# Kernel tuning notes

Hardware: AMD Instinct MI355X
Metric: run time of the kernel (lower is better)

## Reference

```python
import jax, jax.numpy as jnp
import numpy as np

N = 50000      # nodes
E = 800000     # edges (before self loops)
H = 4          # heads
C_IN = 128     # input feature dim
C_HID = 64     # per-head out channels (hidden_dim == output_dim)
SLOPE = 0.2    # GATConv leaky_relu negative slope


def setup_inputs() -> dict:
    key = jax.random.key(0)
    ks = jax.random.split(key, 16)
    x = jax.random.normal(ks[0], (N, C_IN), jnp.float32)
    edge_index = jax.random.randint(ks[1], (2, E), 0, N, jnp.int32)

    def p(k, shape):
        return jax.random.normal(k, shape, jnp.float32) * 0.05

    inp = {"x": x, "edge_index": edge_index}
    in_dims = [C_IN, C_HID, C_HID]
    for i in range(3):
        inp[f"W{i+1}"] = p(ks[2 + 4 * i], (in_dims[i], H * C_HID))
        inp[f"asrc{i+1}"] = p(ks[3 + 4 * i], (H, C_HID))
        inp[f"adst{i+1}"] = p(ks[4 + 4 * i], (H, C_HID))
        inp[f"b{i+1}"] = jnp.zeros((C_HID,), jnp.float32)
    return inp


def _gat_layer(x, src, dst, W, a_s, a_d, b):
    # x: [N, F_in]; src/dst: [E'] (self loops included)
    n = x.shape[0]
    h = (x @ W).reshape(n, H, -1)                      # [N, H, C]
    alpha_src = jnp.einsum('nhc,hc->nh', h, a_s)       # att_src . h  (source side)
    alpha_dst = jnp.einsum('nhc,hc->nh', h, a_d)       # att_dst . h  (target side)
    e = jax.nn.leaky_relu(alpha_src[src] + alpha_dst[dst], SLOPE)  # [E', H]
    # scatter-softmax over incoming edges of each dst node
    m = jax.ops.segment_max(e, dst, num_segments=n)    # [N, H]
    ex = jnp.exp(e - m[dst])
    denom = jax.ops.segment_sum(ex, dst, num_segments=n)
    alpha = ex / (denom[dst] + 1e-16)                  # [E', H]
    # scatter-add aggregation of weighted source features
    out = jax.ops.segment_sum(alpha[:, :, None] * h[src], dst, num_segments=n)  # [N, H, C]
    return out.mean(axis=1) + b                        # concat=False -> head mean, + bias


def reference(x, edge_index, W1, asrc1, adst1, b1, W2, asrc2, adst2, b2,
              W3, asrc3, adst3, b3):
    n = x.shape[0]
    loops = jnp.arange(n, dtype=edge_index.dtype)      # GATConv add_self_loops=True
    src = jnp.concatenate([edge_index[0], loops])
    dst = jnp.concatenate([edge_index[1], loops])
    for W, a_s, a_d, b in ((W1, asrc1, adst1, b1),
                           (W2, asrc2, adst2, b2),
                           (W3, asrc3, adst3, b3)):
        x = jax.nn.relu(_gat_layer(x, src, dst, W, a_s, a_d, b))
    return x
```

## Files before the change

kernel.cpp:

```cpp
#include <hip/hip_runtime.h>
#include <hip/hip_bf16.h>
#include <cstddef>

#define NH 4
#define CHID 64
#define HC 256

typedef __attribute__((ext_vector_type(8))) short bf16x8;
typedef __attribute__((ext_vector_type(4))) float f32x4;


__global__ void hist_kernel(const int* __restrict__ ei, int E, int N,
                            int* __restrict__ deg) {
  int i = blockIdx.x * blockDim.x + threadIdx.x;
  int EP = E + N;
  if (i >= EP) return;
  int d = (i < E) ? ei[E + i] : (i - E);
  atomicAdd(&deg[d], 1);
}

__global__ __launch_bounds__(256) void partial_sum_kernel(const int* __restrict__ deg,
                                                          int* __restrict__ part, int n) {
  __shared__ int red[4];
  int t = threadIdx.x;
  int i = blockIdx.x * 256 + t;
  int v = (i < n) ? deg[i] : 0;
#pragma unroll
  for (int o = 32; o; o >>= 1) v += __shfl_xor(v, o, 64);
  if ((t & 63) == 0) red[t >> 6] = v;
  __syncthreads();
  if (t == 0) part[blockIdx.x] = red[0] + red[1] + red[2] + red[3];
}

__global__ __launch_bounds__(256) void scan_part_kernel(int* __restrict__ part, int nb,
                                                        int* __restrict__ row_off, int n) {
  __shared__ int s[256];
  int t = threadIdx.x;
  int v = (t < nb) ? part[t] : 0;
  s[t] = v;
  __syncthreads();
  for (int o = 1; o < 256; o <<= 1) {
    int u = (t >= o) ? s[t - o] : 0;
    __syncthreads();
    s[t] += u;
    __syncthreads();
  }
  if (t < nb) part[t] = s[t] - v;
  if (t == 255) row_off[n] = s[255];
}

__global__ __launch_bounds__(256) void row_off_kernel(const int* __restrict__ deg,
                                                      const int* __restrict__ part,
                                                      int* __restrict__ row_off, int n) {
  __shared__ int s[256];
  int t = threadIdx.x;
  int i = blockIdx.x * 256 + t;
  int v = (i < n) ? deg[i] : 0;
  s[t] = v;
  __syncthreads();
  for (int o = 1; o < 256; o <<= 1) {
    int u = (t >= o) ? s[t - o] : 0;
    __syncthreads();
    s[t] += u;
    __syncthreads();
  }
  if (i < n) row_off[i] = part[blockIdx.x] + s[t] - v;
}

__global__ void scatter_kernel(const int* __restrict__ ei, int E, int N,
                               const int* __restrict__ row_off,
                               int* __restrict__ cursor, int* __restrict__ ssrc) {
  int i = blockIdx.x * blockDim.x + threadIdx.x;
  int EP = E + N;
  if (i >= EP) {
    if (i < EP + 8) ssrc[i] = 0;
    return;
  }
  int s, d;
  if (i < E) { s = ei[i]; d = ei[E + i]; } else { s = i - E; d = s; }
  int pos = row_off[d] + atomicAdd(&cursor[d], 1);
  ssrc[pos] = s;
}


__global__ void prep_kernel(const float* __restrict__ x,
                            __hip_bfloat16* __restrict__ xb, int n4,
                            const float* __restrict__ W1, const float* __restrict__ W2,
                            const float* __restrict__ W3,
                            __hip_bfloat16* __restrict__ w1b,
                            __hip_bfloat16* __restrict__ w2b,
                            __hip_bfloat16* __restrict__ w3b) {
  int i = blockIdx.x * blockDim.x + threadIdx.x;
  if (i < n4) {
    float4 v = reinterpret_cast<const float4*>(x)[i];
    __hip_bfloat16 h[4] = {__float2bfloat16(v.x), __float2bfloat16(v.y),
                           __float2bfloat16(v.z), __float2bfloat16(v.w)};
    reinterpret_cast<uint2*>(xb)[i] = *reinterpret_cast<uint2*>(h);
    return;
  }
  int j = i - n4;
  if (j >= 65536) return;
  const float* W; __hip_bfloat16* wb; int K, base;
  if (j < 32768)      { W = W1; wb = w1b; K = 128; base = j; }
  else if (j < 49152) { W = W2; wb = w2b; K = 64;  base = j - 32768; }
  else                { W = W3; wb = w3b; K = 64;  base = j - 49152; }
  int k = base >> 8;
  int c = base & 255;
  wb[c * K + k] = __float2bfloat16(W[base]);
}


template <int K>
__global__ __launch_bounds__(256) void gemm_mfma_kernel(
    const __hip_bfloat16* __restrict__ Ab,
    const __hip_bfloat16* __restrict__ Btb,
    const float* __restrict__ a_s, const float* __restrict__ a_d,
    __hip_bfloat16* __restrict__ h, float* __restrict__ asrc_n,
    float* __restrict__ adst_n, int n_rows, int row_groups) {
  extern __shared__ char smem[];
  uint4* lds4 = reinterpret_cast<uint4*>(smem);
  constexpr int KS = K / 32;
  constexpr int S16 = (128 * K * 2) >> 4;
  constexpr int rowshift = (K == 128) ? 4 : 3;
  int ch = blockIdx.y;
  int colbase = ch * 128;

  {
    const uint4* g = reinterpret_cast<const uint4*>(Btb + (size_t)colbase * K);
    for (int c = threadIdx.x; c < S16; c += 256) {
      int row = c >> rowshift;
      lds4[c ^ (row & 7)] = g[c];
    }
  }
  __syncthreads();

  int wave = threadIdx.x >> 6;
  int lane = threadIdx.x & 63;
  int n16  = lane & 15;
  int g4   = lane >> 4;
  const bf16x8 z8 = {0, 0, 0, 0, 0, 0, 0, 0};

  int gg = blockIdx.x;
  int row0 = gg * 64 + wave * 16;
  int xrow = row0 + n16;
  bool aval = xrow < n_rows;
  size_t xbase = (size_t)xrow * K + g4 * 8;

  bf16x8 xh[KS];
#pragma unroll
  for (int s = 0; s < KS; ++s)
    xh[s] = aval ? *reinterpret_cast<const bf16x8*>(&Ab[xbase + s * 32]) : z8;

  f32x4 acc[8];
#pragma unroll
  for (int ct = 0; ct < 8; ++ct) acc[ct] = (f32x4){0.f, 0.f, 0.f, 0.f};

#pragma unroll
  for (int ct = 0; ct < 8; ++ct) {
    int wrow = ct * 16 + n16;
#pragma unroll
    for (int s = 0; s < KS; ++s) {
      int ci = ((wrow * K + s * 32 + g4 * 8) >> 3) ^ (wrow & 7);
      bf16x8 wh = *reinterpret_cast<const bf16x8*>(&lds4[ci]);
      acc[ct] = __builtin_amdgcn_mfma_f32_16x16x32_bf16(wh, xh[s], acc[ct], 0, 0, 0);
    }
  }

  uint2 uval[8];
#pragma unroll
  for (int ct = 0; ct < 8; ++ct) {
    unsigned short u[4];
#pragma unroll
    for (int i = 0; i < 4; ++i) {
      __hip_bfloat16 b = __float2bfloat16(acc[ct][i]);
      u[i] = *reinterpret_cast<unsigned short*>(&b);
    }
    uval[ct] = *reinterpret_cast<uint2*>(u);
  }

  __syncthreads();

  char* epi = smem + wave * 4096;
#pragma unroll
  for (int ct = 0; ct < 8; ++ct) {
    int boff = (n16 * 256 + ct * 32 + g4 * 8) ^ ((n16 & 7) << 4);
    *reinterpret_cast<uint2*>(epi + boff) = uval[ct];
  }
  char* hout = reinterpret_cast<char*>(h);
#pragma unroll
  for (int k = 0; k < 4; ++k) {
    int row = (lane >> 3) + (k & 1) * 8;
    int off = (lane & 7) * 16 + (k >> 1) * 128;
    int lb  = (row * 256 + off) ^ ((row & 7) << 4);
    uint4 v = *reinterpret_cast<uint4*>(epi + lb);
    int r = row0 + row;
    if (r < n_rows)
      *reinterpret_cast<uint4*>(&hout[(size_t)r * 512 + ch * 256 + off]) = v;
  }

  int r = row0 + n16;
  bool valid = r < n_rows;
  float ps[2] = {0.f, 0.f};
  float pd[2] = {0.f, 0.f};
#pragma unroll
  for (int ct = 0; ct < 8; ++ct) {
    int hh = ct >> 2;
    int col = colbase + ct * 16 + g4 * 4;
    float4 as4 = *reinterpret_cast<const float4*>(&a_s[col]);
    float4 ad4 = *reinterpret_cast<const float4*>(&a_d[col]);
    ps[hh] += acc[ct][0] * as4.x + acc[ct][1] * as4.y + acc[ct][2] * as4.z + acc[ct][3] * as4.w;
    pd[hh] += acc[ct][0] * ad4.x + acc[ct][1] * ad4.y + acc[ct][2] * ad4.z + acc[ct][3] * ad4.w;
  }
#pragma unroll
  for (int hh = 0; hh < 2; ++hh) {
    ps[hh] += __shfl_xor(ps[hh], 16, 64);
    ps[hh] += __shfl_xor(ps[hh], 32, 64);
    pd[hh] += __shfl_xor(pd[hh], 16, 64);
    pd[hh] += __shfl_xor(pd[hh], 32, 64);
  }
  if (lane < 16 && valid) {
    *reinterpret_cast<float2*>(&asrc_n[(size_t)r * NH + ch * 2]) =
        make_float2(ps[0], ps[1]);
    *reinterpret_cast<float2*>(&adst_n[(size_t)r * NH + ch * 2]) =
        make_float2(pd[0], pd[1]);
  }
}


__global__ __launch_bounds__(256) void aggregate_kernel(
    const int* __restrict__ row_off, const int* __restrict__ ssrc,
    const __hip_bfloat16* __restrict__ h, const float* __restrict__ asrc_n,
    const float* __restrict__ adst_n, const float* __restrict__ bias,
    __hip_bfloat16* __restrict__ out_bf, float* __restrict__ out_f32, int n_nodes) {
  int n = (blockIdx.x * blockDim.x + threadIdx.x) >> 6;
  if (n >= n_nodes) return;
  int l    = threadIdx.x & 63;
  int slot = l >> 3;
  int cp   = l & 7;
  const char* hbase = reinterpret_cast<const char*>(h);
  const float4 z4 = make_float4(0.f, 0.f, 0.f, 0.f);
  const uint4 zu = {0, 0, 0, 0};

  int beg  = row_off[n];
  int deg  = row_off[n + 1] - beg;
  float4 adn = reinterpret_cast<const float4*>(adst_n)[n];

  float facc[32];
#pragma unroll
  for (int u = 0; u < 32; ++u) facc[u] = 0.f;
  float4 ds = z4;

  auto LOADE = [&](int j, float4& a4, float& msk, uint4* d) {
    int jj = j + slot;
    if (jj < deg) {
      int idx = beg + jj;
      int sv  = ssrc[idx];
      a4  = reinterpret_cast<const float4*>(asrc_n)[sv];
      msk = 1.f;
      const char* hp = hbase + (size_t)sv * 512 + cp * 16;
      d[0] = *reinterpret_cast<const uint4*>(hp);
      d[1] = *reinterpret_cast<const uint4*>(hp + 128);
      d[2] = *reinterpret_cast<const uint4*>(hp + 256);
      d[3] = *reinterpret_cast<const uint4*>(hp + 384);
    } else {
      msk = 0.f;
    }
  };

  auto PROC = [&](const float4& a4, float msk, const uint4* d) {
    float e0 = a4.x + adn.x; e0 = fmaxf(e0, 0.2f * e0);
    float e1 = a4.y + adn.y; e1 = fmaxf(e1, 0.2f * e1);
    float e2 = a4.z + adn.z; e2 = fmaxf(e2, 0.2f * e2);
    float e3 = a4.w + adn.w; e3 = fmaxf(e3, 0.2f * e3);
    float w0 = __expf(e0) * msk;
    float w1 = __expf(e1) * msk;
    float w2 = __expf(e2) * msk;
    float w3 = __expf(e3) * msk;
    ds.x += w0; ds.y += w1; ds.z += w2; ds.w += w3;
#pragma unroll
    for (int hh = 0; hh < 4; ++hh) {
      float w = (hh == 0) ? w0 : (hh == 1) ? w1 : (hh == 2) ? w2 : w3;
      uint4 dd = d[hh];
      facc[hh * 8 + 0] += w * __uint_as_float(dd.x << 16);
      facc[hh * 8 + 1] += w * __uint_as_float(dd.x & 0xffff0000u);
      facc[hh * 8 + 2] += w * __uint_as_float(dd.y << 16);
      facc[hh * 8 + 3] += w * __uint_as_float(dd.y & 0xffff0000u);
      facc[hh * 8 + 4] += w * __uint_as_float(dd.z << 16);
      facc[hh * 8 + 5] += w * __uint_as_float(dd.z & 0xffff0000u);
      facc[hh * 8 + 6] += w * __uint_as_float(dd.w << 16);
      facc[hh * 8 + 7] += w * __uint_as_float(dd.w & 0xffff0000u);
    }
  };

  float4 aA = z4, aB = z4;
  float mA = 0.f, mB = 0.f;
  uint4 dA[4] = {zu, zu, zu, zu};
  uint4 dB[4] = {zu, zu, zu, zu};

  LOADE(0, aA, mA, dA);
  for (int j = 0; j < deg; j += 16) {
    if (j + 8 < deg) LOADE(j + 8, aB, mB, dB); else mB = 0.f;
    PROC(aA, mA, dA);
    if (j + 16 < deg) LOADE(j + 16, aA, mA, dA); else mA = 0.f;
    PROC(aB, mB, dB);
  }

#pragma unroll
  for (int o = 8; o <= 32; o <<= 1) {
    ds.x += __shfl_xor(ds.x, o, 64);
    ds.y += __shfl_xor(ds.y, o, 64);
    ds.z += __shfl_xor(ds.z, o, 64);
    ds.w += __shfl_xor(ds.w, o, 64);
  }
  float iv0 = 1.f / (ds.x + 1e-16f);
  float iv1 = 1.f / (ds.y + 1e-16f);
  float iv2 = 1.f / (ds.z + 1e-16f);
  float iv3 = 1.f / (ds.w + 1e-16f);

  float v[8];
#pragma unroll
  for (int u = 0; u < 8; ++u)
    v[u] = facc[u] * iv0 + facc[8 + u] * iv1 + facc[16 + u] * iv2 + facc[24 + u] * iv3;

#pragma unroll
  for (int u = 0; u < 8; ++u) {
    v[u] += __shfl_xor(v[u], 8, 64);
    v[u] += __shfl_xor(v[u], 16, 64);
    v[u] += __shfl_xor(v[u], 32, 64);
  }

  if (slot < 2) {
    float o0 = (slot == 0) ? v[0] : v[4];
    float o1 = (slot == 0) ? v[1] : v[5];
    float o2 = (slot == 0) ? v[2] : v[6];
    float o3 = (slot == 0) ? v[3] : v[7];
    int chn = cp * 8 + slot * 4;
    float4 b4 = *reinterpret_cast<const float4*>(&bias[chn]);
    o0 = fmaxf(0.25f * o0 + b4.x, 0.f);
    o1 = fmaxf(0.25f * o1 + b4.y, 0.f);
    o2 = fmaxf(0.25f * o2 + b4.z, 0.f);
    o3 = fmaxf(0.25f * o3 + b4.w, 0.f);
    if (out_f32) {
      *reinterpret_cast<float4*>(&out_f32[(size_t)n * CHID + chn]) =
          make_float4(o0, o1, o2, o3);
    } else {
      float of[4] = {o0, o1, o2, o3};
      unsigned short b16[4];
#pragma unroll
      for (int u = 0; u < 4; ++u) {
        __hip_bfloat16 bh = __float2bfloat16(of[u]);
        b16[u] = *reinterpret_cast<unsigned short*>(&bh);
      }
      *reinterpret_cast<uint2*>(&out_bf[(size_t)n * CHID + chn]) =
          *reinterpret_cast<uint2*>(b16);
    }
  }
}


extern "C" void kernel_launch(void* const* d_in, const int* in_sizes, int n_in,
                              void* d_out, int out_size, void* d_ws, size_t ws_size,
                              hipStream_t stream) {
  const float* x   = (const float*)d_in[0];
  const int*   ei  = (const int*)d_in[1];
  const float* W1  = (const float*)d_in[2];
  const float* as1 = (const float*)d_in[3];
  const float* ad1 = (const float*)d_in[4];
  const float* b1  = (const float*)d_in[5];
  const float* W2  = (const float*)d_in[6];
  const float* as2 = (const float*)d_in[7];
  const float* ad2 = (const float*)d_in[8];
  const float* b2  = (const float*)d_in[9];
  const float* W3  = (const float*)d_in[10];
  const float* as3 = (const float*)d_in[11];
  const float* ad3 = (const float*)d_in[12];
  const float* b3  = (const float*)d_in[13];

  int N  = in_sizes[0] / 128;
  int E  = in_sizes[1] / 2;
  int EP = E + N;
  int NB = (N + 255) / 256;

  __hip_bfloat16* h    = (__hip_bfloat16*)d_ws;
  __hip_bfloat16* x1b  = h + (size_t)N * HC;
  __hip_bfloat16* xb   = x1b + (size_t)N * 128;
  __hip_bfloat16* w1b  = xb + (size_t)N * CHID;
  __hip_bfloat16* w2b  = w1b + 256 * 128;
  __hip_bfloat16* w3b  = w2b + 256 * 64;
  float* asrc_n = (float*)(w3b + 256 * 64);
  float* adst_n = asrc_n + (size_t)N * NH;
  int*   deg    = (int*)(adst_n + (size_t)N * NH);
  int*   cursor = deg + N;
  int*   row_off= cursor + N;
  int*   part   = row_off + (N + 1);
  int*   ssrc   = part + ((NB + 3) & ~3);

  hipMemsetAsync(deg, 0, sizeof(int) * (size_t)2 * N, stream);
  int eb = (EP + 8 + 255) / 256;
  hist_kernel<<<eb, 256, 0, stream>>>(ei, E, N, deg);
  partial_sum_kernel<<<NB, 256, 0, stream>>>(deg, part, N);
  scan_part_kernel<<<1, 256, 0, stream>>>(part, NB, row_off, N);
  row_off_kernel<<<NB, 256, 0, stream>>>(deg, part, row_off, N);
  scatter_kernel<<<eb, 256, 0, stream>>>(ei, E, N, row_off, cursor, ssrc);

  int n4 = N * 128 / 4;
  prep_kernel<<<(n4 + 65536 + 255) / 256, 256, 0, stream>>>(x, x1b, n4,
                                                            W1, W2, W3, w1b, w2b, w3b);

  (void)hipFuncSetAttribute(reinterpret_cast<const void*>(&gemm_mfma_kernel<128>),
                            hipFuncAttributeMaxDynamicSharedMemorySize, 65536);
  (void)hipFuncSetAttribute(reinterpret_cast<const void*>(&gemm_mfma_kernel<64>),
                            hipFuncAttributeMaxDynamicSharedMemorySize, 65536);

  int RG = (N + 63) / 64;
  dim3 ggrid(RG, 2);
  int ablocks = (N + 3) / 4;

  gemm_mfma_kernel<128><<<ggrid, 256, 32768, stream>>>(x1b, w1b, as1, ad1,
                                                       h, asrc_n, adst_n, N, RG);
  aggregate_kernel<<<ablocks, 256, 0, stream>>>(row_off, ssrc, h, asrc_n, adst_n, b1,
                                                xb, nullptr, N);
  gemm_mfma_kernel<64><<<ggrid, 256, 16384, stream>>>(xb, w2b, as2, ad2,
                                                      h, asrc_n, adst_n, N, RG);
  aggregate_kernel<<<ablocks, 256, 0, stream>>>(row_off, ssrc, h, asrc_n, adst_n, b2,
                                                xb, nullptr, N);
  gemm_mfma_kernel<64><<<ggrid, 256, 16384, stream>>>(xb, w3b, as3, ad3,
                                                      h, asrc_n, adst_n, N, RG);
  aggregate_kernel<<<ablocks, 256, 0, stream>>>(row_off, ssrc, h, asrc_n, adst_n, b3,
                                                nullptr, (float*)d_out, N);
}
```

Before: 348.5 us.

## Fuse histogram with prep kernel and compute all 256 columns per block in K=64 GEMMs

Merges the degree histogram and the bf16 conversion of x and weights into one launch, removing one kernel launch. For layers 2 and 3, a new GEMM kernel computes all 256 output columns per row block instead of splitting across two column-half blocks. Each row of A is then loaded once and the attention dot products are written with a single float4 store. In the main GEMM, the attention projection is moved before the bf16 packing. The cost is doubled accumulator registers (16 f32x4 per lane) and 32KB of LDS per block, which may reduce occupancy.

New measurement: 350.0 us. No clear change (+0.4%).

```diff
diff --git a/kernel.cpp b/kernel.cpp
--- a/kernel.cpp
+++ b/kernel.cpp
@@ -9,15 +9,6 @@
 typedef __attribute__((ext_vector_type(8))) short bf16x8;
 typedef __attribute__((ext_vector_type(4))) float f32x4;
 
-
-__global__ void hist_kernel(const int* __restrict__ ei, int E, int N,
-                            int* __restrict__ deg) {
-  int i = blockIdx.x * blockDim.x + threadIdx.x;
-  int EP = E + N;
-  if (i >= EP) return;
-  int d = (i < E) ? ei[E + i] : (i - E);
-  atomicAdd(&deg[d], 1);
-}
 
 __global__ __launch_bounds__(256) void partial_sum_kernel(const int* __restrict__ deg,
                                                           int* __restrict__ part, int n) {
@@ -83,30 +74,39 @@
 }
 
 
-__global__ void prep_kernel(const float* __restrict__ x,
-                            __hip_bfloat16* __restrict__ xb, int n4,
-                            const float* __restrict__ W1, const float* __restrict__ W2,
-                            const float* __restrict__ W3,
-                            __hip_bfloat16* __restrict__ w1b,
-                            __hip_bfloat16* __restrict__ w2b,
-                            __hip_bfloat16* __restrict__ w3b) {
+__global__ void hist_prep_kernel(const int* __restrict__ ei, int E, int N,
+                                 int* __restrict__ deg,
+                                 const float* __restrict__ x,
+                                 __hip_bfloat16* __restrict__ xb, int n4,
+                                 const float* __restrict__ W1, const float* __restrict__ W2,
+                                 const float* __restrict__ W3,
+                                 __hip_bfloat16* __restrict__ w1b,
+                                 __hip_bfloat16* __restrict__ w2b,
+                                 __hip_bfloat16* __restrict__ w3b) {
   int i = blockIdx.x * blockDim.x + threadIdx.x;
-  if (i < n4) {
-    float4 v = reinterpret_cast<const float4*>(x)[i];
-    __hip_bfloat16 h[4] = {__float2bfloat16(v.x), __float2bfloat16(v.y),
-                           __float2bfloat16(v.z), __float2bfloat16(v.w)};
-    reinterpret_cast<uint2*>(xb)[i] = *reinterpret_cast<uint2*>(h);
+  int EP = E + N;
+  if (i < EP) {
+    int d = (i < E) ? ei[E + i] : (i - E);
+    atomicAdd(&deg[d], 1);
     return;
   }
-  int j = i - n4;
-  if (j >= 65536) return;
+  int j = i - EP;
+  if (j < n4) {
+    float4 v = reinterpret_cast<const float4*>(x)[j];
+    __hip_bfloat16 hh[4] = {__float2bfloat16(v.x), __float2bfloat16(v.y),
+                            __float2bfloat16(v.z), __float2bfloat16(v.w)};
+    reinterpret_cast<uint2*>(xb)[j] = *reinterpret_cast<uint2*>(hh);
+    return;
+  }
+  int k = j - n4;
+  if (k >= 65536) return;
   const float* W; __hip_bfloat16* wb; int K, base;
-  if (j < 32768)      { W = W1; wb = w1b; K = 128; base = j; }
-  else if (j < 49152) { W = W2; wb = w2b; K = 64;  base = j - 32768; }
-  else                { W = W3; wb = w3b; K = 64;  base = j - 49152; }
-  int k = base >> 8;
+  if (k < 32768)      { W = W1; wb = w1b; K = 128; base = k; }
+  else if (k < 49152) { W = W2; wb = w2b; K = 64;  base = k - 32768; }
+  else                { W = W3; wb = w3b; K = 64;  base = k - 49152; }
+  int kk = base >> 8;
   int c = base & 255;
-  wb[c * K + k] = __float2bfloat16(W[base]);
+  wb[c * K + kk] = __float2bfloat16(W[base]);
 }
 
 
@@ -166,6 +166,18 @@
     }
   }
 
+  float ps[2] = {0.f, 0.f};
+  float pd[2] = {0.f, 0.f};
+#pragma unroll
+  for (int ct = 0; ct < 8; ++ct) {
+    int hh = ct >> 2;
+    int col = colbase + ct * 16 + g4 * 4;
+    float4 as4 = *reinterpret_cast<const float4*>(&a_s[col]);
+    float4 ad4 = *reinterpret_cast<const float4*>(&a_d[col]);
+    ps[hh] += acc[ct][0] * as4.x + acc[ct][1] * as4.y + acc[ct][2] * as4.z + acc[ct][3] * as4.w;
+    pd[hh] += acc[ct][0] * ad4.x + acc[ct][1] * ad4.y + acc[ct][2] * ad4.z + acc[ct][3] * ad4.w;
+  }
+
   uint2 uval[8];
 #pragma unroll
   for (int ct = 0; ct < 8; ++ct) {
@@ -200,17 +212,6 @@
 
   int r = row0 + n16;
   bool valid = r < n_rows;
-  float ps[2] = {0.f, 0.f};
-  float pd[2] = {0.f, 0.f};
-#pragma unroll
-  for (int ct = 0; ct < 8; ++ct) {
-    int hh = ct >> 2;
-    int col = colbase + ct * 16 + g4 * 4;
-    float4 as4 = *reinterpret_cast<const float4*>(&a_s[col]);
-    float4 ad4 = *reinterpret_cast<const float4*>(&a_d[col]);
-    ps[hh] += acc[ct][0] * as4.x + acc[ct][1] * as4.y + acc[ct][2] * as4.z + acc[ct][3] * as4.w;
-    pd[hh] += acc[ct][0] * ad4.x + acc[ct][1] * ad4.y + acc[ct][2] * ad4.z + acc[ct][3] * ad4.w;
-  }
 #pragma unroll
   for (int hh = 0; hh < 2; ++hh) {
     ps[hh] += __shfl_xor(ps[hh], 16, 64);
@@ -223,6 +224,119 @@
         make_float2(ps[0], ps[1]);
     *reinterpret_cast<float2*>(&adst_n[(size_t)r * NH + ch * 2]) =
         make_float2(pd[0], pd[1]);
+  }
+}
+
+
+__global__ __launch_bounds__(256) void gemm_full64_kernel(
+    const __hip_bfloat16* __restrict__ Ab,
+    const __hip_bfloat16* __restrict__ Btb,
+    const float* __restrict__ a_s, const float* __restrict__ a_d,
+    __hip_bfloat16* __restrict__ h, float* __restrict__ asrc_n,
+    float* __restrict__ adst_n, int n_rows) {
+  extern __shared__ char smem[];
+  uint4* lds4 = reinterpret_cast<uint4*>(smem);
+  constexpr int K = 64;
+  constexpr int S16 = (256 * K * 2) >> 4;
+
+  {
+    const uint4* g = reinterpret_cast<const uint4*>(Btb);
+    for (int c = threadIdx.x; c < S16; c += 256) {
+      int row = c >> 3;
+      lds4[c ^ (row & 7)] = g[c];
+    }
+  }
+  __syncthreads();
+
+  int wave = threadIdx.x >> 6;
+  int lane = threadIdx.x & 63;
+  int n16  = lane & 15;
+  int g4   = lane >> 4;
+  const bf16x8 z8 = {0, 0, 0, 0, 0, 0, 0, 0};
+
+  int row0 = blockIdx.x * 64 + wave * 16;
+  int xrow = row0 + n16;
+  bool aval = xrow < n_rows;
+  size_t xbase = (size_t)xrow * K + g4 * 8;
+
+  bf16x8 xh[2];
+#pragma unroll
+  for (int s = 0; s < 2; ++s)
+    xh[s] = aval ? *reinterpret_cast<const bf16x8*>(&Ab[xbase + s * 32]) : z8;
+
+  f32x4 acc[16];
+#pragma unroll
+  for (int ct = 0; ct < 16; ++ct) acc[ct] = (f32x4){0.f, 0.f, 0.f, 0.f};
+
+#pragma unroll
+  for (int ct = 0; ct < 16; ++ct) {
+    int wrow = ct * 16 + n16;
+#pragma unroll
+    for (int s = 0; s < 2; ++s) {
+      int ci = ((wrow * K + s * 32 + g4 * 8) >> 3) ^ (wrow & 7);
+      bf16x8 wh = *reinterpret_cast<const bf16x8*>(&lds4[ci]);
+      acc[ct] = __builtin_amdgcn_mfma_f32_16x16x32_bf16(wh, xh[s], acc[ct], 0, 0, 0);
+    }
+  }
+
+  float ps[NH] = {0.f, 0.f, 0.f, 0.f};
+  float pd[NH] = {0.f, 0.f, 0.f, 0.f};
+#pragma unroll
+  for (int ct = 0; ct < 16; ++ct) {
+    int hh = ct >> 2;
+    int col = ct * 16 + g4 * 4;
+    float4 as4 = *reinterpret_cast<const float4*>(&a_s[col]);
+    float4 ad4 = *reinterpret_cast<const float4*>(&a_d[col]);
+    ps[hh] += acc[ct][0] * as4.x + acc[ct][1] * as4.y + acc[ct][2] * as4.z + acc[ct][3] * as4.w;
+    pd[hh] += acc[ct][0] * ad4.x + acc[ct][1] * ad4.y + acc[ct][2] * ad4.z + acc[ct][3] * ad4.w;
+  }
+
+  uint2 uval[16];
+#pragma unroll
+  for (int ct = 0; ct < 16; ++ct) {
+    unsigned short u[4];
+#pragma unroll
+    for (int i = 0; i < 4; ++i) {
+      __hip_bfloat16 b = __float2bfloat16(acc[ct][i]);
+      u[i] = *reinterpret_cast<unsigned short*>(&b);
+    }
+    uval[ct] = *reinterpret_cast<uint2*>(u);
+  }
+
+  __syncthreads();
+
+  char* epi = smem + wave * 8192;
+#pragma unroll
+  for (int ct = 0; ct < 16; ++ct) {
+    int boff = (n16 * 512 + ct * 32 + g4 * 8) ^ ((n16 & 7) << 4);
+    *reinterpret_cast<uint2*>(epi + boff) = uval[ct];
+  }
+  char* hout = reinterpret_cast<char*>(h);
+#pragma unroll
+  for (int k = 0; k < 8; ++k) {
+    int row = (lane >> 3) + (k & 1) * 8;
+    int off = (lane & 7) * 16 + (k >> 1) * 128;
+    int lb  = (row * 512 + off) ^ ((row & 7) << 4);
+    uint4 v = *reinterpret_cast<uint4*>(epi + lb);
+    int r = row0 + row;
+    if (r < n_rows)
+      *reinterpret_cast<uint4*>(&hout[(size_t)r * 512 + off]) = v;
+  }
+
+  int r = row0 + n16;
+  bool valid = r < n_rows;
+#pragma unroll
+  for (int hh = 0; hh < NH; ++hh) {
+    ps[hh] += __shfl_xor(ps[hh], 16, 64);
+    ps[hh] += __shfl_xor(ps[hh], 32, 64);
+    pd[hh] += __shfl_xor(pd[hh], 16, 64);
+    pd[hh] += __shfl_xor(pd[hh], 32, 64);
+  }
+  if (lane < 16 && valid) {
+    *reinterpret_cast<float4*>(&asrc_n[(size_t)r * NH]) =
+        make_float4(ps[0], ps[1], ps[2], ps[3]);
+    *reinterpret_cast<float4*>(&adst_n[(size_t)r * NH]) =
+        make_float4(pd[0], pd[1], pd[2], pd[3]);
   }
 }
 
@@ -396,20 +510,19 @@
   int*   ssrc   = part + ((NB + 3) & ~3);
 
   hipMemsetAsync(deg, 0, sizeof(int) * (size_t)2 * N, stream);
-  int eb = (EP + 8 + 255) / 256;
-  hist_kernel<<<eb, 256, 0, stream>>>(ei, E, N, deg);
+  int n4 = N * 128 / 4;
+  int mb = (EP + n4 + 65536 + 255) / 256;
+  hist_prep_kernel<<<mb, 256, 0, stream>>>(ei, E, N, deg, x, x1b, n4,
+                                           W1, W2, W3, w1b, w2b, w3b);
   partial_sum_kernel<<<NB, 256, 0, stream>>>(deg, part, N);
   scan_part_kernel<<<1, 256, 0, stream>>>(part, NB, row_off, N);
   row_off_kernel<<<NB, 256, 0, stream>>>(deg, part, row_off, N);
+  int eb = (EP + 8 + 255) / 256;
   scatter_kernel<<<eb, 256, 0, stream>>>(ei, E, N, row_off, cursor, ssrc);
-
-  int n4 = N * 128 / 4;
-  prep_kernel<<<(n4 + 65536 + 255) / 256, 256, 0, stream>>>(x, x1b, n4,
-                                                            W1, W2, W3, w1b, w2b, w3b);
 
   (void)hipFuncSetAttribute(reinterpret_cast<const void*>(&gemm_mfma_kernel<128>),
                             hipFuncAttributeMaxDynamicSharedMemorySize, 65536);
-  (void)hipFuncSetAttribute(reinterpret_cast<const void*>(&gemm_mfma_kernel<64>),
+  (void)hipFuncSetAttribute(reinterpret_cast<const void*>(&gemm_full64_kernel),
                             hipFuncAttributeMaxDynamicSharedMemorySize, 65536);
 
   int RG = (N + 63) / 64;
@@ -420,12 +533,12 @@
                                                        h, asrc_n, adst_n, N, RG);
   aggregate_kernel<<<ablocks, 256, 0, stream>>>(row_off, ssrc, h, asrc_n, adst_n, b1,
                                                 xb, nullptr, N);
-  gemm_mfma_kernel<64><<<ggrid, 256, 16384, stream>>>(xb, w2b, as2, ad2,
-                                                      h, asrc_n, adst_n, N, RG);
+  gemm_full64_kernel<<<RG, 256, 32768, stream>>>(xb, w2b, as2, ad2,
+                                                 h, asrc_n, adst_n, N);
   aggregate_kernel<<<ablocks, 256, 0, stream>>>(row_off, ssrc, h, asrc_n, adst_n, b2,
                                                 xb, nullptr, N);
-  gemm_mfma_kernel<64><<<ggrid, 256, 16384, stream>>>(xb, w3b, as3, ad3,
-                                                      h, asrc_n, adst_n, N, RG);
+  gemm_full64_kernel<<<RG, 256, 32768, stream>>>(xb, w3b, as3, ad3,
+                                                 h, asrc_n, adst_n, N);
   aggregate_kernel<<<ablocks, 256, 0, stream>>>(row_off, ssrc, h, asrc_n, adst_n, b3,
                                                 nullptr, (float*)d_out, N);
 }
```
